# Kernel tuning notes

Hardware: AMD Instinct MI355X
Metric: run time of the kernel (lower is better)

Reference implementation:

```python
import jax, jax.numpy as jnp
import numpy as np

B, S, F, H, P, O = 512, 336, 16, 256, 48, 1

def _gru_cell(x, h, Wih, Whh, bih, bhh):
    # torch GRU gate order: r, z, n
    gx = x @ Wih.T + bih            # [B, 3H]
    gh = h @ Whh.T + bhh            # [B, 3H]
    rx, zx, nx = jnp.split(gx, 3, axis=-1)
    rh, zh, nh = jnp.split(gh, 3, axis=-1)
    r = jax.nn.sigmoid(rx + rh)
    z = jax.nn.sigmoid(zx + zh)
    n = jnp.tanh(nx + r * nh)
    return (1.0 - z) * n + z * h

def setup_inputs() -> dict:
    key = jax.random.key(0)
    ks = jax.random.split(key, 12)
    s = lambda *sh: 1.0 / np.sqrt(sh[-1])
    d = {}
    d["xb"] = jax.random.normal(ks[0], (B, S, F), dtype=jnp.float32)
    # encoder GRU (1 layer, unidirectional)
    d["enc_Wih"] = jax.random.normal(ks[1], (3 * H, F), dtype=jnp.float32) * s(F)
    d["enc_Whh"] = jax.random.normal(ks[2], (3 * H, H), dtype=jnp.float32) * s(H)
    d["enc_bih"] = jnp.zeros((3 * H,), dtype=jnp.float32)
    d["enc_bhh"] = jnp.zeros((3 * H,), dtype=jnp.float32)
    # attention linear: (H + F) -> S
    d["att_W"] = jax.random.normal(ks[3], (S, H + F), dtype=jnp.float32) * s(H + F)
    d["att_b"] = jnp.zeros((S,), dtype=jnp.float32)
    # decoder GRUCell: input H, hidden H
    d["dec_Wih"] = jax.random.normal(ks[4], (3 * H, H), dtype=jnp.float32) * s(H)
    d["dec_Whh"] = jax.random.normal(ks[5], (3 * H, H), dtype=jnp.float32) * s(H)
    d["dec_bih"] = jnp.zeros((3 * H,), dtype=jnp.float32)
    d["dec_bhh"] = jnp.zeros((3 * H,), dtype=jnp.float32)
    # decoder output: H -> F
    d["out_W"] = jax.random.normal(ks[6], (F, H), dtype=jnp.float32) * s(H)
    d["out_b"] = jnp.zeros((F,), dtype=jnp.float32)
    # final linear: F -> O
    d["lin_W"] = jax.random.normal(ks[7], (O, F), dtype=jnp.float32) * s(F)
    d["lin_b"] = jnp.zeros((O,), dtype=jnp.float32)
    return d

def reference(xb, enc_Wih, enc_Whh, enc_bih, enc_bhh, att_W, att_b,
              dec_Wih, dec_Whh, dec_bih, dec_bhh, out_W, out_b, lin_W, lin_b):
    # ---- encoder: GRU over time ----
    h0 = jnp.zeros((B, H), dtype=xb.dtype)
    xs = jnp.swapaxes(xb, 0, 1)  # [S, B, F]

    def enc_step(h, x):
        h2 = _gru_cell(x, h, enc_Wih, enc_Whh, enc_bih, enc_bhh)
        return h2, h2

    enc_hidden, enc_out = jax.lax.scan(enc_step, h0, xs)
    enc_out = jnp.swapaxes(enc_out, 0, 1)  # [B, S, H]

    # ---- decoder: per-step attention + GRUCell + output proj ----
    y0 = xb[:, -1, :]  # [B, F]

    def dec_step(carry, _):
        h, y = carry
        att_in = jnp.concatenate([h, y], axis=1)          # [B, H+F]
        attn = jax.nn.softmax(att_in @ att_W.T + att_b, axis=-1)  # [B, S]
        combine = jnp.einsum('bs,bsh->bh', attn, enc_out)  # [B, H]
        h2 = _gru_cell(combine, h, dec_Wih, dec_Whh, dec_bih, dec_bhh)
        out = h2 @ out_W.T + out_b                         # [B, F]
        return (h2, out), out

    _, outs = jax.lax.scan(dec_step, (enc_hidden, y0), None, length=P)  # [P, B, F]
    outs = jnp.swapaxes(outs, 0, 1)                        # [B, P, F]
    outs = outs @ lin_W.T + lin_b                          # [B, P, O]
    return outs.squeeze(-1)                                # [B, P]
```

## Files before the change

### kernel.cpp

```cpp
#include <hip/hip_runtime.h>
#include <cstdint>
#include <cstddef>

#define B_ 512
#define S_ 336
#define F_ 16
#define H_ 256
#define P_ 48

typedef __bf16 bhalf;
typedef __attribute__((ext_vector_type(8))) __bf16 bhalf8;
typedef __attribute__((ext_vector_type(4))) float f32x4;

#define MFMA16(A, Bv, C) __builtin_amdgcn_mfma_f32_16x16x32_bf16((A), (Bv), (C), 0, 0, 0)

__device__ __forceinline__ float fastrcp(float x) { return __builtin_amdgcn_rcpf(x); }
__device__ __forceinline__ float sigm(float x) { return fastrcp(1.0f + __expf(-x)); }
__device__ __forceinline__ float tanh_f(float x) { return 2.0f * fastrcp(1.0f + __expf(-2.0f * x)) - 1.0f; }

__device__ __forceinline__ bhalf u16_to_bf(unsigned int u) {
  return __builtin_bit_cast(__bf16, (unsigned short)u);
}
__device__ __forceinline__ unsigned short bf_to_u16(bhalf b) {
  return __builtin_bit_cast(unsigned short, b);
}

__device__ __forceinline__ bhalf8 bzero8() {
  bhalf8 v;
#pragma unroll
  for (int j = 0; j < 8; ++j) v[j] = (bhalf)0.0f;
  return v;
}

__global__ __launch_bounds__(128, 1) void enc_kernel(
    const float* __restrict__ Whh, const float* __restrict__ Wih,
    const float* __restrict__ bih, const float* __restrict__ bhh,
    const float* __restrict__ xb,
    bhalf* __restrict__ enc_out,
    float* __restrict__ hcur,
    unsigned int* __restrict__ hpack,
    unsigned int* __restrict__ flags)
{
  __shared__ bhalf lds_lo[54 * 64 * 8];
  const bhalf8* lds_v = (const bhalf8*)lds_lo;

  const int tid  = threadIdx.x;
  const int lane = tid & 63;
  const int wv   = tid >> 6;
  const int ncol = lane & 15;
  const int quad = lane >> 4;

  const int blk = blockIdx.x;
  const int g   = (blk & 7) * 4 + (blk >> 6);
  const int w   = (blk >> 3) & 7;
  const int b0  = g * 16;
  const int iw0 = w * 32;
  const int i0  = iw0 + wv * 16;

  for (int it = tid; it < 54 * 64; it += 128) {
    const int fi = it >> 6;
    const int ln = it & 63;
    const int kt = fi % 9;
    const int rem = fi / 9;
    const int gg = rem % 3;
    const int wv2 = rem / 3;
    const int jrow = gg * 256 + iw0 + wv2 * 16 + (ln & 15);
    const int kbase = kt * 32 + ((ln >> 4) << 3);
    bhalf* dst = lds_lo + (size_t)it * 8;
#pragma unroll
    for (int j = 0; j < 8; ++j) {
      const int k = kbase + j;
      float v = 0.0f;
      if (k < 256) v = Whh[(size_t)jrow * 256 + k];
      else if (k < 272) v = Wih[(size_t)jrow * 16 + (k - 256)];
      const bhalf hi = (bhalf)v;
      dst[j] = (bhalf)(v - (float)hi);
    }
  }

  bhalf8 bWh[3][9];
#pragma unroll
  for (int gg = 0; gg < 3; ++gg) {
    const int jrow = gg * 256 + i0 + ncol;
#pragma unroll
    for (int kt = 0; kt < 9; ++kt) {
      bhalf8 v = bzero8();
      if (kt < 8) {
        const float* src = Whh + (size_t)jrow * 256 + kt * 32 + quad * 8;
#pragma unroll
        for (int j = 0; j < 8; ++j) v[j] = (bhalf)src[j];
      } else if (quad < 2) {
        const float* src = Wih + (size_t)jrow * 16 + quad * 8;
#pragma unroll
        for (int j = 0; j < 8; ++j) v[j] = (bhalf)src[j];
      }
      bWh[gg][kt] = v;
    }
  }

  const int jr = i0 + ncol;
  const float bR  = bih[jr]       + bhh[jr];
  const float bZ  = bih[256 + jr] + bhh[256 + jr];
  const float bNx = bih[512 + jr];
  const float bNh = bhh[512 + jr];

  __syncthreads();

  const int bA = b0 + ncol;
  const int kA = quad * 8;

  float hold[4] = {0.0f, 0.0f, 0.0f, 0.0f};

  for (int t = 0; t < S_; ++t) {
    bhalf8 xh = bzero8(), xl = bzero8();
    if (quad < 2) {
      const float* xp = xb + ((size_t)bA * S_ + t) * F_ + quad * 8;
#pragma unroll
      for (int j = 0; j < 8; ++j) {
        const float v = xp[j];
        const bhalf h = (bhalf)v;
        xh[j] = h;
        xl[j] = (bhalf)(v - (float)h);
      }
    }

    if (t > 0) {
      unsigned int* fp = &flags[g * S_ + (t - 1)];
      if (tid == 0) {
        while (__hip_atomic_load(fp, __ATOMIC_RELAXED, __HIP_MEMORY_SCOPE_AGENT) < 8u)
          __builtin_amdgcn_s_sleep(1);
      }
      __syncthreads();
    }

    f32x4 aR0 = {0,0,0,0}, aR1 = {0,0,0,0}, aR2 = {0,0,0,0};
    f32x4 aZ0 = {0,0,0,0}, aZ1 = {0,0,0,0}, aZ2 = {0,0,0,0};
    f32x4 aN0 = {0,0,0,0}, aN1 = {0,0,0,0}, aN2 = {0,0,0,0};
    f32x4 aNx = {0,0,0,0};

    if (t > 0) {
      const int slot = (t - 1) & 1;
      const unsigned long long* hp64 =
          (const unsigned long long*)(hpack + ((size_t)slot * B_ + bA) * H_ + kA);
#pragma unroll
      for (int kt = 0; kt < 8; ++kt) {
        bhalf8 Ah, Al;
#pragma unroll
        for (int j2 = 0; j2 < 4; ++j2) {
          const unsigned long long w2 =
              __hip_atomic_load(hp64 + kt * 16 + j2, __ATOMIC_RELAXED,
                                __HIP_MEMORY_SCOPE_AGENT);
          Ah[2 * j2]     = u16_to_bf((unsigned int)w2);
          Al[2 * j2]     = u16_to_bf((unsigned int)(w2 >> 16));
          Ah[2 * j2 + 1] = u16_to_bf((unsigned int)(w2 >> 32));
          Al[2 * j2 + 1] = u16_to_bf((unsigned int)(w2 >> 48));
        }
        const bhalf8 wl0 = lds_v[((wv * 3 + 0) * 9 + kt) * 64 + lane];
        const bhalf8 wl1 = lds_v[((wv * 3 + 1) * 9 + kt) * 64 + lane];
        const bhalf8 wl2 = lds_v[((wv * 3 + 2) * 9 + kt) * 64 + lane];
        aR0 = MFMA16(Ah, bWh[0][kt], aR0);
        aR1 = MFMA16(Ah, wl0, aR1);
        aR2 = MFMA16(Al, bWh[0][kt], aR2);
        aZ0 = MFMA16(Ah, bWh[1][kt], aZ0);
        aZ1 = MFMA16(Ah, wl1, aZ1);
        aZ2 = MFMA16(Al, bWh[1][kt], aZ2);
        aN0 = MFMA16(Ah, bWh[2][kt], aN0);
        aN1 = MFMA16(Ah, wl2, aN1);
        aN2 = MFMA16(Al, bWh[2][kt], aN2);
      }
    }
    {
      const bhalf8 wl0 = lds_v[((wv * 3 + 0) * 9 + 8) * 64 + lane];
      const bhalf8 wl1 = lds_v[((wv * 3 + 1) * 9 + 8) * 64 + lane];
      const bhalf8 wl2 = lds_v[((wv * 3 + 2) * 9 + 8) * 64 + lane];
      aR0 = MFMA16(xh, bWh[0][8], aR0);
      aR1 = MFMA16(xh, wl0, aR1);
      aR2 = MFMA16(xl, bWh[0][8], aR2);
      aZ0 = MFMA16(xh, bWh[1][8], aZ0);
      aZ1 = MFMA16(xh, wl1, aZ1);
      aZ2 = MFMA16(xl, bWh[1][8], aZ2);
      aNx = MFMA16(xh, bWh[2][8], aNx);
      aNx = MFMA16(xh, wl2, aNx);
      aNx = MFMA16(xl, bWh[2][8], aNx);
    }

    const int iL = i0 + ncol;
    bhalf his[4], los[4];
#pragma unroll
    for (int r = 0; r < 4; ++r) {
      const float sR  = aR0[r] + aR1[r] + aR2[r] + bR;
      const float sZ  = aZ0[r] + aZ1[r] + aZ2[r] + bZ;
      const float nhv = aN0[r] + aN1[r] + aN2[r] + bNh;
      const float nxv = aNx[r] + bNx;
      const float rr = sigm(sR);
      const float zz = sigm(sZ);
      const float nn = tanh_f(nxv + rr * nhv);
      const float h2 = (1.0f - zz) * nn + zz * hold[r];
      hold[r] = h2;
      his[r] = (bhalf)h2;
      los[r] = (bhalf)(h2 - (float)his[r]);
      const int bb = b0 + quad * 4 + r;
      const unsigned int wrd =
          (unsigned int)bf_to_u16(his[r]) | ((unsigned int)bf_to_u16(los[r]) << 16);
      __hip_atomic_store(&hpack[((size_t)(t & 1) * B_ + bb) * H_ + iL], wrd,
                         __ATOMIC_RELAXED, __HIP_MEMORY_SCOPE_AGENT);
    }

    __syncthreads();
    if (tid == 0) {
      __hip_atomic_fetch_add(&flags[g * S_ + t], 1u, __ATOMIC_RELAXED,
                             __HIP_MEMORY_SCOPE_AGENT);
    }

#pragma unroll
    for (int r = 0; r < 4; ++r) {
      const int bb = b0 + quad * 4 + r;
      enc_out[((size_t)bb * S_ + t) * H_ + iL] = his[r];
    }
  }

#pragma unroll
  for (int r = 0; r < 4; ++r)
    hcur[(size_t)(b0 + quad * 4 + r) * H_ + i0 + ncol] = hold[r];
}

__global__ __launch_bounds__(256) void wpack_kernel(const float* __restrict__ Whh,
                                                    const float* __restrict__ Wih,
                                                    bhalf* __restrict__ wbT) {
  const int idx = blockIdx.x * 256 + threadIdx.x;
  if (idx >= 64 * 768 * 8) return;
  const int j = idx & 7;
  const int row = (idx >> 3) % 768;
  const int k8 = idx / (768 * 8);
  const int k = k8 * 8 + j;
  const float v = (k < 256) ? Whh[(size_t)row * 256 + k]
                            : Wih[(size_t)row * 256 + (k - 256)];
  wbT[idx] = (bhalf)v;
}

__global__ __launch_bounds__(256) void apack_kernel(const float* __restrict__ attW,
                                                    bhalf* __restrict__ abT) {
  const int idx = blockIdx.x * 256 + threadIdx.x;
  if (idx >= 36 * 336 * 8) return;
  const int j = idx & 7;
  const int s = (idx >> 3) % 336;
  const int k8 = idx / (8 * 336);
  const int k = k8 * 8 + j;
  abT[idx] = (k < 272) ? (bhalf)attW[(size_t)s * 272 + k] : (bhalf)0.0f;
}

__global__ __launch_bounds__(256) void dec_kernel(
    const bhalf* __restrict__ wbT,
    const bhalf* __restrict__ abT,
    const float* __restrict__ attb,
    const float* __restrict__ bih, const float* __restrict__ bhh,
    const float* __restrict__ outW, const float* __restrict__ outb,
    const float* __restrict__ linW, const float* __restrict__ linb,
    const bhalf* __restrict__ enc_out, const float* __restrict__ hcur,
    const float* __restrict__ xb, float* __restrict__ dout)
{
  __shared__ __align__(16) bhalf encL[126 * 256];
  __shared__ float hyL[288];
  __shared__ float cL[256];
  __shared__ float sc[S_];
  __shared__ float pC[8][32][9];
  __shared__ float oP[4][16];
  __shared__ float oF[16];
  __shared__ float red[8];
  const int tid  = threadIdx.x;
  const int lane = tid & 63;
  const int wv   = tid >> 6;
  const int b    = blockIdx.x;
  const int jj   = tid;
  const int cg   = tid & 31;
  const int ck   = tid >> 5;

  {
    const bhalf8* src = (const bhalf8*)(enc_out + (size_t)b * S_ * H_);
    bhalf8* dst = (bhalf8*)encL;
    for (int it = tid; it < 126 * 32; it += 256) dst[it] = src[it];
  }

  hyL[tid] = hcur[(size_t)b * H_ + tid];
  if (tid < 16) hyL[256 + tid] = xb[((size_t)b * S_ + (S_ - 1)) * F_ + tid];
  else if (tid < 32) hyL[256 + tid] = 0.0f;

  const float bRv  = bih[jj]       + bhh[jj];
  const float bZv  = bih[256 + jj] + bhh[256 + jj];
  const float bNxv = bih[512 + jj];
  const float bNhv = bhh[512 + jj];

  const bhalf* epC = enc_out + ((size_t)b * S_ + ck * 42) * H_ + cg * 8;
  const bhalf* epL = encL + (size_t)(ck * 42) * H_ + cg * 8;
  __syncthreads();

  for (int p = 0; p < P_; ++p) {
    for (int s = tid; s < S_; s += 256) {
      float d0 = 0, d1 = 0, d2 = 0, d3 = 0;
#pragma unroll 4
      for (int k8 = 0; k8 < 36; ++k8) {
        const bhalf8 q = *(const bhalf8*)(abT + ((size_t)k8 * S_ + s) * 8);
        const float* v = hyL + k8 * 8;
        d0 += (float)q[0] * v[0] + (float)q[4] * v[4];
        d1 += (float)q[1] * v[1] + (float)q[5] * v[5];
        d2 += (float)q[2] * v[2] + (float)q[6] * v[6];
        d3 += (float)q[3] * v[3] + (float)q[7] * v[7];
      }
      sc[s] = d0 + d1 + d2 + d3 + attb[s];
    }
    __syncthreads();

    float mx = -3e38f;
    for (int s = tid; s < S_; s += 256) mx = fmaxf(mx, sc[s]);
#pragma unroll
    for (int o = 32; o > 0; o >>= 1) mx = fmaxf(mx, __shfl_xor(mx, o, 64));
    if (lane == 0) red[wv] = mx;
    __syncthreads();
    mx = fmaxf(fmaxf(red[0], red[1]), fmaxf(red[2], red[3]));
    float sum = 0.0f;
    for (int s = tid; s < S_; s += 256) {
      const float e = __expf(sc[s] - mx);
      sc[s] = e;
      sum += e;
    }
#pragma unroll
    for (int o = 32; o > 0; o >>= 1) sum += __shfl_xor(sum, o, 64);
    if (lane == 0) red[4 + wv] = sum;
    __syncthreads();
    const float inv = fastrcp(red[4] + red[5] + red[6] + red[7]);
    for (int s = tid; s < S_; s += 256) sc[s] *= inv;
    __syncthreads();

    {
      float a0 = 0, a1 = 0, a2 = 0, a3 = 0, a4 = 0, a5 = 0, a6 = 0, a7 = 0;
      const float* scrow = sc + ck * 42;
      if (ck < 3) {
#pragma unroll 6
        for (int s5 = 0; s5 < 42; ++s5) {
          const bhalf8 v = *(const bhalf8*)(epL + (size_t)s5 * H_);
          const float wgt = scrow[s5];
          a0 += wgt * (float)v[0];
          a1 += wgt * (float)v[1];
          a2 += wgt * (float)v[2];
          a3 += wgt * (float)v[3];
          a4 += wgt * (float)v[4];
          a5 += wgt * (float)v[5];
          a6 += wgt * (float)v[6];
          a7 += wgt * (float)v[7];
        }
      } else {
#pragma unroll 6
        for (int s5 = 0; s5 < 42; ++s5) {
          const bhalf8 v = *(const bhalf8*)(epC + (size_t)s5 * H_);
          const float wgt = scrow[s5];
          a0 += wgt * (float)v[0];
          a1 += wgt * (float)v[1];
          a2 += wgt * (float)v[2];
          a3 += wgt * (float)v[3];
          a4 += wgt * (float)v[4];
          a5 += wgt * (float)v[5];
          a6 += wgt * (float)v[6];
          a7 += wgt * (float)v[7];
        }
      }
      float* pp = pC[ck][cg];
      pp[0] = a0; pp[1] = a1; pp[2] = a2; pp[3] = a3;
      pp[4] = a4; pp[5] = a5; pp[6] = a6; pp[7] = a7;
    }
    __syncthreads();
    {
      float s = 0.0f;
      const int gg = jj >> 3, j = jj & 7;
#pragma unroll
      for (int c = 0; c < 8; ++c) s += pC[c][gg][j];
      cL[jj] = s;
    }
    __syncthreads();

    float hnew;
    {
      float r0 = 0, r1 = 0, z0 = 0, z1 = 0, nh0 = 0, nh1 = 0, nx0 = 0, nx1 = 0;
#pragma unroll 4
      for (int k8 = 0; k8 < 32; ++k8) {
        const bhalf* base = wbT + ((size_t)k8 * 768) * 8;
        const bhalf8 qR = *(const bhalf8*)(base + (size_t)jj * 8);
        const bhalf8 qZ = *(const bhalf8*)(base + (size_t)(256 + jj) * 8);
        const bhalf8 qN = *(const bhalf8*)(base + (size_t)(512 + jj) * 8);
        const float* v = hyL + k8 * 8;
        r0 += (float)qR[0]*v[0] + (float)qR[2]*v[2] + (float)qR[4]*v[4] + (float)qR[6]*v[6];
        r1 += (float)qR[1]*v[1] + (float)qR[3]*v[3] + (float)qR[5]*v[5] + (float)qR[7]*v[7];
        z0 += (float)qZ[0]*v[0] + (float)qZ[2]*v[2] + (float)qZ[4]*v[4] + (float)qZ[6]*v[6];
        z1 += (float)qZ[1]*v[1] + (float)qZ[3]*v[3] + (float)qZ[5]*v[5] + (float)qZ[7]*v[7];
        nh0 += (float)qN[0]*v[0] + (float)qN[2]*v[2] + (float)qN[4]*v[4] + (float)qN[6]*v[6];
        nh1 += (float)qN[1]*v[1] + (float)qN[3]*v[3] + (float)qN[5]*v[5] + (float)qN[7]*v[7];
      }
#pragma unroll 4
      for (int k8 = 32; k8 < 64; ++k8) {
        const bhalf* base = wbT + ((size_t)k8 * 768) * 8;
        const bhalf8 qR = *(const bhalf8*)(base + (size_t)jj * 8);
        const bhalf8 qZ = *(const bhalf8*)(base + (size_t)(256 + jj) * 8);
        const bhalf8 qN = *(const bhalf8*)(base + (size_t)(512 + jj) * 8);
        const float* v = cL + (k8 - 32) * 8;
        r0 += (float)qR[0]*v[0] + (float)qR[2]*v[2] + (float)qR[4]*v[4] + (float)qR[6]*v[6];
        r1 += (float)qR[1]*v[1] + (float)qR[3]*v[3] + (float)qR[5]*v[5] + (float)qR[7]*v[7];
        z0 += (float)qZ[0]*v[0] + (float)qZ[2]*v[2] + (float)qZ[4]*v[4] + (float)qZ[6]*v[6];
        z1 += (float)qZ[1]*v[1] + (float)qZ[3]*v[3] + (float)qZ[5]*v[5] + (float)qZ[7]*v[7];
        nx0 += (float)qN[0]*v[0] + (float)qN[2]*v[2] + (float)qN[4]*v[4] + (float)qN[6]*v[6];
        nx1 += (float)qN[1]*v[1] + (float)qN[3]*v[3] + (float)qN[5]*v[5] + (float)qN[7]*v[7];
      }
      const float sR = r0 + r1 + bRv;
      const float sZ = z0 + z1 + bZv;
      const float nh = nh0 + nh1 + bNhv;
      const float nx = nx0 + nx1 + bNxv;
      const float rr = 1.0f / (1.0f + __expf(-sR));
      const float zz = 1.0f / (1.0f + __expf(-sZ));
      const float nn = tanhf(nx + rr * nh);
      hnew = (1.0f - zz) * nn + zz * hyL[jj];
    }
    __syncthreads();
    hyL[jj] = hnew;
    __syncthreads();

    if (tid < 64) {
      const int f = tid & 15, q = tid >> 4;
      const float* wr = outW + (size_t)f * H_ + q * 64;
      const float* hv = hyL + q * 64;
      float a0 = 0, a1 = 0, a2 = 0, a3 = 0;
#pragma unroll 4
      for (int k = 0; k < 64; k += 4) {
        a0 += wr[k]     * hv[k];
        a1 += wr[k + 1] * hv[k + 1];
        a2 += wr[k + 2] * hv[k + 2];
        a3 += wr[k + 3] * hv[k + 3];
      }
      oP[q][f] = a0 + a1 + a2 + a3;
    }
    __syncthreads();
    if (tid < 16) {
      const float o = oP[0][tid] + oP[1][tid] + oP[2][tid] + oP[3][tid] + outb[tid];
      oF[tid] = o;
      hyL[256 + tid] = o;
    }
    __syncthreads();
    if (tid == 0) {
      float pr = linb[0];
#pragma unroll
      for (int f = 0; f < 16; ++f) pr += oF[f] * linW[f];
      dout[(size_t)b * P_ + p] = pr;
    }
  }
}

extern "C" void kernel_launch(void* const* d_in, const int* in_sizes, int n_in,
                              void* d_out, int out_size, void* d_ws, size_t ws_size,
                              hipStream_t stream)
{
  (void)in_sizes; (void)n_in; (void)out_size;
  const float* xb      = (const float*)d_in[0];
  const float* enc_Wih = (const float*)d_in[1];
  const float* enc_Whh = (const float*)d_in[2];
  const float* enc_bih = (const float*)d_in[3];
  const float* enc_bhh = (const float*)d_in[4];
  const float* att_W   = (const float*)d_in[5];
  const float* att_b   = (const float*)d_in[6];
  const float* dec_Wih = (const float*)d_in[7];
  const float* dec_Whh = (const float*)d_in[8];
  const float* dec_bih = (const float*)d_in[9];
  const float* dec_bhh = (const float*)d_in[10];
  const float* out_W   = (const float*)d_in[11];
  const float* out_b   = (const float*)d_in[12];
  const float* lin_W   = (const float*)d_in[13];
  const float* lin_b   = (const float*)d_in[14];
  float* dout = (float*)d_out;

  char* ws = (char*)d_ws;
  const size_t off_enc = 0;
  const size_t off_hp  = off_enc + (size_t)B_ * S_ * H_ * 2;
  const size_t off_hc  = off_hp + (size_t)2 * B_ * H_ * 4;
  const size_t off_wb  = off_hc + (size_t)B_ * H_ * 4;
  const size_t off_ab  = off_wb + (size_t)64 * 768 * 8 * 2;
  const size_t off_fl  = off_ab + (size_t)36 * 336 * 8 * 2;
  const size_t need    = off_fl + 32 * S_ * sizeof(unsigned int);
  if (ws_size < need) return;

  bhalf* enc_out      = (bhalf*)(ws + off_enc);
  unsigned int* hpack = (unsigned int*)(ws + off_hp);
  float* hcur         = (float*)(ws + off_hc);
  bhalf* wbT          = (bhalf*)(ws + off_wb);
  bhalf* abT          = (bhalf*)(ws + off_ab);
  unsigned int* flags = (unsigned int*)(ws + off_fl);

  (void)hipMemsetAsync(flags, 0, 32 * S_ * sizeof(unsigned int), stream);
  wpack_kernel<<<(64 * 768 * 8 + 255) / 256, 256, 0, stream>>>(dec_Whh, dec_Wih, wbT);
  apack_kernel<<<(36 * 336 * 8 + 255) / 256, 256, 0, stream>>>(att_W, abT);
  enc_kernel<<<256, 128, 0, stream>>>(enc_Whh, enc_Wih, enc_bih, enc_bhh, xb,
                                      enc_out, hcur, hpack, flags);
  dec_kernel<<<B_, 256, 0, stream>>>(wbT, abT, att_b, dec_bih, dec_bhh,
                                     out_W, out_b, lin_W, lin_b,
                                     enc_out, hcur, xb, dout);
}
```

Baseline: 3.170 ms.

## Keep encoder weight residuals in registers and use per-block step flags

The low-part bf16 weight residuals move from LDS into registers, so the MFMA loop no longer issues LDS loads. Inter-block sync changes from per-step fetch-add counters (tid0 spin plus __syncthreads) to one monotonic step counter per block. Every wave polls the 8 producer flags directly, one per lane. The input-projection MFMAs are issued before the wait so they overlap the spin. The cost is roughly doubled register use for weights, which risks spills at this launch bound, and more polling traffic.

```diff
diff --git a/kernel.cpp b/kernel.cpp
--- a/kernel.cpp
+++ b/kernel.cpp
@@ -41,9 +41,6 @@
     unsigned int* __restrict__ hpack,
     unsigned int* __restrict__ flags)
 {
-  __shared__ bhalf lds_lo[54 * 64 * 8];
-  const bhalf8* lds_v = (const bhalf8*)lds_lo;
-
   const int tid  = threadIdx.x;
   const int lane = tid & 63;
   const int wv   = tid >> 6;
@@ -57,44 +54,34 @@
   const int iw0 = w * 32;
   const int i0  = iw0 + wv * 16;
 
-  for (int it = tid; it < 54 * 64; it += 128) {
-    const int fi = it >> 6;
-    const int ln = it & 63;
-    const int kt = fi % 9;
-    const int rem = fi / 9;
-    const int gg = rem % 3;
-    const int wv2 = rem / 3;
-    const int jrow = gg * 256 + iw0 + wv2 * 16 + (ln & 15);
-    const int kbase = kt * 32 + ((ln >> 4) << 3);
-    bhalf* dst = lds_lo + (size_t)it * 8;
-#pragma unroll
-    for (int j = 0; j < 8; ++j) {
-      const int k = kbase + j;
-      float v = 0.0f;
-      if (k < 256) v = Whh[(size_t)jrow * 256 + k];
-      else if (k < 272) v = Wih[(size_t)jrow * 16 + (k - 256)];
-      const bhalf hi = (bhalf)v;
-      dst[j] = (bhalf)(v - (float)hi);
-    }
-  }
-
-  bhalf8 bWh[3][9];
+  bhalf8 bWh[3][9], bWl[3][9];
 #pragma unroll
   for (int gg = 0; gg < 3; ++gg) {
     const int jrow = gg * 256 + i0 + ncol;
 #pragma unroll
     for (int kt = 0; kt < 9; ++kt) {
-      bhalf8 v = bzero8();
+      bhalf8 vh = bzero8(), vl = bzero8();
       if (kt < 8) {
         const float* src = Whh + (size_t)jrow * 256 + kt * 32 + quad * 8;
 #pragma unroll
-        for (int j = 0; j < 8; ++j) v[j] = (bhalf)src[j];
+        for (int j = 0; j < 8; ++j) {
+          const float v = src[j];
+          const bhalf h = (bhalf)v;
+          vh[j] = h;
+          vl[j] = (bhalf)(v - (float)h);
+        }
       } else if (quad < 2) {
         const float* src = Wih + (size_t)jrow * 16 + quad * 8;
 #pragma unroll
-        for (int j = 0; j < 8; ++j) v[j] = (bhalf)src[j];
-      }
-      bWh[gg][kt] = v;
+        for (int j = 0; j < 8; ++j) {
+          const float v = src[j];
+          const bhalf h = (bhalf)v;
+          vh[j] = h;
+          vl[j] = (bhalf)(v - (float)h);
+        }
+      }
+      bWh[gg][kt] = vh;
+      bWl[gg][kt] = vl;
     }
   }
 
@@ -104,8 +91,6 @@
   const float bNx = bih[512 + jr];
   const float bNh = bhh[512 + jr];
 
-  __syncthreads();
-
   const int bA = b0 + ncol;
   const int kA = quad * 8;
 
@@ -124,21 +109,27 @@
       }
     }
 
-    if (t > 0) {
-      unsigned int* fp = &flags[g * S_ + (t - 1)];
-      if (tid == 0) {
-        while (__hip_atomic_load(fp, __ATOMIC_RELAXED, __HIP_MEMORY_SCOPE_AGENT) < 8u)
-          __builtin_amdgcn_s_sleep(1);
-      }
-      __syncthreads();
-    }
-
     f32x4 aR0 = {0,0,0,0}, aR1 = {0,0,0,0}, aR2 = {0,0,0,0};
     f32x4 aZ0 = {0,0,0,0}, aZ1 = {0,0,0,0}, aZ2 = {0,0,0,0};
     f32x4 aN0 = {0,0,0,0}, aN1 = {0,0,0,0}, aN2 = {0,0,0,0};
     f32x4 aNx = {0,0,0,0};
 
+    aR0 = MFMA16(xh, bWh[0][8], aR0);
+    aR1 = MFMA16(xh, bWl[0][8], aR1);
+    aR2 = MFMA16(xl, bWh[0][8], aR2);
+    aZ0 = MFMA16(xh, bWh[1][8], aZ0);
+    aZ1 = MFMA16(xh, bWl[1][8], aZ1);
+    aZ2 = MFMA16(xl, bWh[1][8], aZ2);
+    aNx = MFMA16(xh, bWh[2][8], aNx);
+    aNx = MFMA16(xh, bWl[2][8], aNx);
+    aNx = MFMA16(xl, bWh[2][8], aNx);
+
     if (t > 0) {
+      const unsigned int* fp = &flags[g * 8 + (lane & 7)];
+      while (__hip_atomic_load(fp, __ATOMIC_RELAXED, __HIP_MEMORY_SCOPE_AGENT) <
+             (unsigned int)t)
+        __builtin_amdgcn_s_sleep(1);
+
       const int slot = (t - 1) & 1;
       const unsigned long long* hp64 =
           (const unsigned long long*)(hpack + ((size_t)slot * B_ + bA) * H_ + kA);
@@ -155,37 +146,20 @@
           Ah[2 * j2 + 1] = u16_to_bf((unsigned int)(w2 >> 32));
           Al[2 * j2 + 1] = u16_to_bf((unsigned int)(w2 >> 48));
         }
-        const bhalf8 wl0 = lds_v[((wv * 3 + 0) * 9 + kt) * 64 + lane];
-        const bhalf8 wl1 = lds_v[((wv * 3 + 1) * 9 + kt) * 64 + lane];
-        const bhalf8 wl2 = lds_v[((wv * 3 + 2) * 9 + kt) * 64 + lane];
         aR0 = MFMA16(Ah, bWh[0][kt], aR0);
-        aR1 = MFMA16(Ah, wl0, aR1);
+        aR1 = MFMA16(Ah, bWl[0][kt], aR1);
         aR2 = MFMA16(Al, bWh[0][kt], aR2);
         aZ0 = MFMA16(Ah, bWh[1][kt], aZ0);
-        aZ1 = MFMA16(Ah, wl1, aZ1);
+        aZ1 = MFMA16(Ah, bWl[1][kt], aZ1);
         aZ2 = MFMA16(Al, bWh[1][kt], aZ2);
         aN0 = MFMA16(Ah, bWh[2][kt], aN0);
-        aN1 = MFMA16(Ah, wl2, aN1);
+        aN1 = MFMA16(Ah, bWl[2][kt], aN1);
         aN2 = MFMA16(Al, bWh[2][kt], aN2);
       }
     }
-    {
-      const bhalf8 wl0 = lds_v[((wv * 3 + 0) * 9 + 8) * 64 + lane];
-      const bhalf8 wl1 = lds_v[((wv * 3 + 1) * 9 + 8) * 64 + lane];
-      const bhalf8 wl2 = lds_v[((wv * 3 + 2) * 9 + 8) * 64 + lane];
-      aR0 = MFMA16(xh, bWh[0][8], aR0);
-      aR1 = MFMA16(xh, wl0, aR1);
-      aR2 = MFMA16(xl, bWh[0][8], aR2);
-      aZ0 = MFMA16(xh, bWh[1][8], aZ0);
-      aZ1 = MFMA16(xh, wl1, aZ1);
-      aZ2 = MFMA16(xl, bWh[1][8], aZ2);
-      aNx = MFMA16(xh, bWh[2][8], aNx);
-      aNx = MFMA16(xh, wl2, aNx);
-      aNx = MFMA16(xl, bWh[2][8], aNx);
-    }
 
     const int iL = i0 + ncol;
-    bhalf his[4], los[4];
+    bhalf his[4];
 #pragma unroll
     for (int r = 0; r < 4; ++r) {
       const float sR  = aR0[r] + aR1[r] + aR2[r] + bR;
@@ -198,18 +172,18 @@
       const float h2 = (1.0f - zz) * nn + zz * hold[r];
       hold[r] = h2;
       his[r] = (bhalf)h2;
-      los[r] = (bhalf)(h2 - (float)his[r]);
+      const bhalf lo = (bhalf)(h2 - (float)his[r]);
       const int bb = b0 + quad * 4 + r;
       const unsigned int wrd =
-          (unsigned int)bf_to_u16(his[r]) | ((unsigned int)bf_to_u16(los[r]) << 16);
+          (unsigned int)bf_to_u16(his[r]) | ((unsigned int)bf_to_u16(lo) << 16);
       __hip_atomic_store(&hpack[((size_t)(t & 1) * B_ + bb) * H_ + iL], wrd,
                          __ATOMIC_RELAXED, __HIP_MEMORY_SCOPE_AGENT);
     }
 
     __syncthreads();
     if (tid == 0) {
-      __hip_atomic_fetch_add(&flags[g * S_ + t], 1u, __ATOMIC_RELAXED,
-                             __HIP_MEMORY_SCOPE_AGENT);
+      __hip_atomic_store(&flags[g * 8 + w], (unsigned int)(t + 1),
+                         __ATOMIC_RELAXED, __HIP_MEMORY_SCOPE_AGENT);
     }
 
 #pragma unroll
@@ -480,7 +454,7 @@
   const size_t off_wb  = off_hc + (size_t)B_ * H_ * 4;
   const size_t off_ab  = off_wb + (size_t)64 * 768 * 8 * 2;
   const size_t off_fl  = off_ab + (size_t)36 * 336 * 8 * 2;
-  const size_t need    = off_fl + 32 * S_ * sizeof(unsigned int);
+  const size_t need    = off_fl + 32 * 8 * sizeof(unsigned int);
   if (ws_size < need) return;
 
   bhalf* enc_out      = (bhalf*)(ws + off_enc);
@@ -490,7 +464,7 @@
   bhalf* abT          = (bhalf*)(ws + off_ab);
   unsigned int* flags = (unsigned int*)(ws + off_fl);
 
-  (void)hipMemsetAsync(flags, 0, 32 * S_ * sizeof(unsigned int), stream);
+  (void)hipMemsetAsync(flags, 0, 32 * 8 * sizeof(unsigned int), stream);
   wpack_kernel<<<(64 * 768 * 8 + 255) / 256, 256, 0, stream>>>(dec_Whh, dec_Wih, wbT);
   apack_kernel<<<(36 * 336 * 8 + 255) / 256, 256, 0, stream>>>(att_W, abT);
   enc_kernel<<<256, 128, 0, stream>>>(enc_Whh, enc_Wih, enc_bih, enc_bhh, xb,
```

Result: faster. 3.102 ms (-2.1%).
